# Kernel optimization log

Hardware: AMD Instinct MI355X
Metric: run time of the kernel (lower is better)

Reference implementation:

```python
import jax, jax.numpy as jnp
from jax import lax
import numpy as np

INPUT_SIZE = 32
HIDDEN = 128
FC1 = 64
OUT = 1
BATCH = 1024
SEQ = 512


def _lstm_layer(x, w_ih, w_hh, b_ih, b_hh):
    """Single PyTorch-convention LSTM layer (batch_first). x: [B,T,I] -> [B,T,H].
    Gate order in the 4H dim is (i, f, g, o), matching nn.LSTM."""
    B = x.shape[0]
    H = w_hh.shape[1]
    # Precompute input contribution for all timesteps (big GEMM, done once).
    gx = jnp.einsum('bti,gi->btg', x, w_ih) + b_ih + b_hh  # [B,T,4H]
    gx_t = jnp.swapaxes(gx, 0, 1)  # [T,B,4H] for scan over time

    def step(carry, gxt):
        h, c = carry
        gates = gxt + h @ w_hh.T  # [B,4H]
        i, f, g, o = jnp.split(gates, 4, axis=-1)
        i = jax.nn.sigmoid(i)
        f = jax.nn.sigmoid(f)
        g = jnp.tanh(g)
        o = jax.nn.sigmoid(o)
        c = f * c + i * g
        h = o * jnp.tanh(c)
        return (h, c), h

    h0 = jnp.zeros((B, H), dtype=x.dtype)
    c0 = jnp.zeros((B, H), dtype=x.dtype)
    (_, _), hs = lax.scan(step, (h0, c0), gx_t)
    return jnp.swapaxes(hs, 0, 1)  # [B,T,H]


def setup_inputs() -> dict:
    key = jax.random.key(0)
    ks = jax.random.split(key, 16)
    s_in = 1.0 / np.sqrt(HIDDEN)  # PyTorch LSTM init scale
    inp = {
        'x': jax.random.normal(ks[0], (BATCH, SEQ, INPUT_SIZE), dtype=jnp.float32),
        # LSTM layer 0
        'w_ih0': jax.random.uniform(ks[1], (4 * HIDDEN, INPUT_SIZE), minval=-s_in, maxval=s_in),
        'w_hh0': jax.random.uniform(ks[2], (4 * HIDDEN, HIDDEN), minval=-s_in, maxval=s_in),
        'b_ih0': jax.random.uniform(ks[3], (4 * HIDDEN,), minval=-s_in, maxval=s_in),
        'b_hh0': jax.random.uniform(ks[4], (4 * HIDDEN,), minval=-s_in, maxval=s_in),
        # LSTM layer 1
        'w_ih1': jax.random.uniform(ks[5], (4 * HIDDEN, HIDDEN), minval=-s_in, maxval=s_in),
        'w_hh1': jax.random.uniform(ks[6], (4 * HIDDEN, HIDDEN), minval=-s_in, maxval=s_in),
        'b_ih1': jax.random.uniform(ks[7], (4 * HIDDEN,), minval=-s_in, maxval=s_in),
        'b_hh1': jax.random.uniform(ks[8], (4 * HIDDEN,), minval=-s_in, maxval=s_in),
        # FC head
        'fc1_w': jax.random.uniform(ks[9], (FC1, HIDDEN), minval=-s_in, maxval=s_in),
        'fc1_b': jax.random.uniform(ks[10], (FC1,), minval=-s_in, maxval=s_in),
        'fc2_w': jax.random.uniform(ks[11], (OUT, FC1), minval=-1.0 / np.sqrt(FC1), maxval=1.0 / np.sqrt(FC1)),
        'fc2_b': jax.random.uniform(ks[12], (OUT,), minval=-1.0 / np.sqrt(FC1), maxval=1.0 / np.sqrt(FC1)),
    }
    return inp


def reference(x, w_ih0, w_hh0, b_ih0, b_hh0, w_ih1, w_hh1, b_ih1, b_hh1,
              fc1_w, fc1_b, fc2_w, fc2_b):
    # 2-layer LSTM (inter-layer dropout disabled: eval/inference mode)
    h1 = _lstm_layer(x, w_ih0, w_hh0, b_ih0, b_hh0)   # [B,T,H]
    h2 = _lstm_layer(h1, w_ih1, w_hh1, b_ih1, b_hh1)  # [B,T,H]
    last = h2[:, -1, :]                                # [B,H]
    out = jax.nn.relu(last @ fc1_w.T + fc1_b)          # [B,64]; dropout = identity (eval)
    out = out @ fc2_w.T + fc2_b                        # [B,1]
    return out
```

## Files before the change

### kernel.cpp

```cpp
#include <hip/hip_runtime.h>

#define HID   128
#define SEQL  512
#define MT    16
#define TPB   512
#define BATCH 1024

typedef __attribute__((ext_vector_type(4))) float    f32x4;
typedef __attribute__((ext_vector_type(8))) _Float16 f16x8;

union Pack8 { int2 p2[2]; int4 p4; f16x8 h; _Float16 hf[8]; short s[8]; };

__device__ __forceinline__ short f2hs(float f) {
    _Float16 v = (_Float16)f;
    return __builtin_bit_cast(short, v);
}
__device__ __forceinline__ float fsig(float x) {
    return __builtin_amdgcn_rcpf(1.f + __expf(-x));
}
__device__ __forceinline__ float ftanh(float x) {
    return 1.f - 2.f * __builtin_amdgcn_rcpf(1.f + __expf(2.f * x));
}

__global__ void prep_kernel(const float* __restrict__ x,
                            const float* __restrict__ w_ih0, const float* __restrict__ w_hh0,
                            const float* __restrict__ b_ih0, const float* __restrict__ b_hh0,
                            const float* __restrict__ w_ih1, const float* __restrict__ w_hh1,
                            const float* __restrict__ b_ih1, const float* __restrict__ b_hh1,
                            short* __restrict__ recW0, short* __restrict__ recW1,
                            short* __restrict__ inW1, short* __restrict__ xW0,
                            float* __restrict__ bias0, float* __restrict__ bias1,
                            short* __restrict__ xf) {
    int tid = blockIdx.x * 256 + threadIdx.x;
    if (tid < 2097152) {
        int g4 = tid & 3, c = (tid >> 2) & 15, t = (tid >> 6) & 511, grp = tid >> 15;
        const float* src = x + ((size_t)(grp * 16 + c) * 512 + t) * 32 + g4 * 8;
        Pack8 p;
        #pragma unroll
        for (int i = 0; i < 8; ++i) p.hf[i] = (_Float16)src[i];
        *(int4*)(xf + (size_t)tid * 8) = p.p4;
    } else if (tid < 2121728) {
        int q = tid - 2097152;
        int m = q >> 13;
        int r = q & 8191;
        int lane = r & 63, kk = (r >> 6) & 3, g = (r >> 8) & 3, w = r >> 10;
        int c = lane & 15, g4 = lane >> 4;
        int col = g * 128 + w * 16 + c;
        const float* src = (m == 0) ? w_hh0 : (m == 1) ? w_hh1 : w_ih1;
        short* dst = ((m == 0) ? recW0 : (m == 1) ? recW1 : inW1) + (size_t)r * 8;
        #pragma unroll
        for (int i = 0; i < 8; ++i)
            dst[i] = f2hs(src[col * 128 + kk * 32 + 8 * g4 + i]);
    } else if (tid < 2123776) {
        int r = tid - 2121728;
        int lane = r & 63, g = (r >> 6) & 3, w = r >> 8;
        int c = lane & 15, g4 = lane >> 4;
        int col = g * 128 + w * 16 + c;
        short* dst = xW0 + (size_t)r * 8;
        #pragma unroll
        for (int i = 0; i < 8; ++i)
            dst[i] = f2hs(w_ih0[col * 32 + 8 * g4 + i]);
    } else if (tid < 2124288) {
        int j = tid - 2123776;
        bias0[j] = b_ih0[j] + b_hh0[j];
    } else if (tid < 2124800) {
        int j = tid - 2124288;
        bias1[j] = b_ih1[j] + b_hh1[j];
    }
}

__global__ __launch_bounds__(TPB, 2) void fused_lstm_kernel(
    const short* __restrict__ xf,
    const short* __restrict__ recW0g, const short* __restrict__ recW1g,
    const short* __restrict__ inW1g,  const short* __restrict__ xW0g,
    const float* __restrict__ bias0,  const float* __restrict__ bias1,
    const float* __restrict__ fc1_w, const float* __restrict__ fc1_b,
    const float* __restrict__ fc2_w, const float* __restrict__ fc2_b,
    float* __restrict__ out)
{
    extern __shared__ char smem[];
    short* inL = (short*)smem;
    char*  hS0 = smem + 131072;
    char*  hS1 = smem + 139264;

    const int tid = threadIdx.x;
    const int w = tid >> 6, lane = tid & 63;
    const int c = lane & 15, g4 = lane >> 4;
    const int row0 = blockIdx.x * MT;

    #pragma unroll
    for (int i = 0; i < 32; ++i)
        ((int4*)inL)[i * TPB + tid] = ((const int4*)inW1g)[i * TPB + tid];
    #pragma unroll
    for (int i = 0; i < 8; ++i)
        ((int*)hS0)[i * TPB + tid] = 0;

    Pack8 recW0f[4][4], recW1f[4][4], xWf[4];
    #pragma unroll
    for (int g = 0; g < 4; ++g)
        #pragma unroll
        for (int kk = 0; kk < 4; ++kk) {
            recW0f[g][kk].p4 = *(const int4*)(recW0g + (size_t)((((w*4+g)*4+kk)*64 + lane) * 8));
            recW1f[g][kk].p4 = *(const int4*)(recW1g + (size_t)((((w*4+g)*4+kk)*64 + lane) * 8));
        }
    #pragma unroll
    for (int g = 0; g < 4; ++g)
        xWf[g].p4 = *(const int4*)(xW0g + (size_t)(((w*4+g)*64 + lane) * 8));

    float biasr0[4], biasr1[4];
    #pragma unroll
    for (int g = 0; g < 4; ++g) {
        biasr0[g] = bias0[g*128 + w*16 + c];
        biasr1[g] = bias1[g*128 + w*16 + c];
    }

    __syncthreads();

    float cst0[4] = {0.f, 0.f, 0.f, 0.f};
    float cst1[4] = {0.f, 0.f, 0.f, 0.f};

    const short* xfp = xf + (size_t)blockIdx.x * 262144 + c * 32 + g4 * 8;

    const int swz   = (c & 14) << 3;
    const int rbase = c * 256;
    const int unit  = w * 16 + c;
    int woff[4];
    #pragma unroll
    for (int r = 0; r < 4; ++r) {
        int rrow = 4 * g4 + r;
        woff[r] = rrow * 256 + ((unit * 2) ^ ((rrow & 14) << 3));
    }
    const int inBbase = w * 16384;

    Pack8 xv, xn;
    xv.p4 = *(const int4*)(xfp);
    xn.p4 = *(const int4*)(xfp + 512);

    {
        Pack8 ah0[4];
        #pragma unroll
        for (int kk = 0; kk < 4; ++kk)
            ah0[kk].p4 = *(const int4*)(hS0 + (rbase + ((kk*64 + 16*g4) ^ swz)));
        f32x4 acc0[4];
        #pragma unroll
        for (int g = 0; g < 4; ++g) { float b = biasr0[g]; acc0[g] = (f32x4){b,b,b,b}; }
        #pragma unroll
        for (int g = 0; g < 4; ++g)
            acc0[g] = __builtin_amdgcn_mfma_f32_16x16x32_f16(xv.h, xWf[g].h, acc0[g], 0, 0, 0);
        #pragma unroll
        for (int kk = 0; kk < 4; ++kk)
            #pragma unroll
            for (int g = 0; g < 4; ++g)
                acc0[g] = __builtin_amdgcn_mfma_f32_16x16x32_f16(ah0[kk].h, recW0f[g][kk].h, acc0[g], 0, 0, 0);
        char* h0w = hS0 + 4096;
        #pragma unroll
        for (int r = 0; r < 4; ++r) {
            float si = fsig(acc0[0][r]), sf = fsig(acc0[1][r]);
            float tg = ftanh(acc0[2][r]), so = fsig(acc0[3][r]);
            float cc = sf * cst0[r] + si * tg;
            cst0[r] = cc;
            float hh = so * ftanh(cc);
            *(_Float16*)(h0w + woff[r]) = (_Float16)hh;
        }
        __syncthreads();
    }

    for (int t = 1; t < SEQL; ++t) {
        const int rb = t & 1;
        const char* h0r = hS0 + rb * 4096;
        const char* h1r = hS1 + rb * 4096;
        char* h0w = hS0 + (rb ^ 1) * 4096;
        char* h1w = hS1 + (rb ^ 1) * 4096;

        xv = xn;
        int tn = (t + 1 < SEQL) ? t + 1 : SEQL - 1;
        xn.p4 = *(const int4*)(xfp + (size_t)tn * 512);

        Pack8 ah0[4], ah1[4];
        #pragma unroll
        for (int kk = 0; kk < 4; ++kk) {
            ah0[kk].p4 = *(const int4*)(h0r + (rbase + ((kk*64 + 16*g4) ^ swz)));
            ah1[kk].p4 = *(const int4*)(h1r + (rbase + ((kk*64 + 16*g4) ^ swz)));
        }

        __builtin_amdgcn_s_setprio(1);
        f32x4 acc0[4];
        #pragma unroll
        for (int g = 0; g < 4; ++g) { float b = biasr0[g]; acc0[g] = (f32x4){b,b,b,b}; }
        #pragma unroll
        for (int g = 0; g < 4; ++g)
            acc0[g] = __builtin_amdgcn_mfma_f32_16x16x32_f16(xv.h, xWf[g].h, acc0[g], 0, 0, 0);
        #pragma unroll
        for (int kk = 0; kk < 4; ++kk)
            #pragma unroll
            for (int g = 0; g < 4; ++g)
                acc0[g] = __builtin_amdgcn_mfma_f32_16x16x32_f16(ah0[kk].h, recW0f[g][kk].h, acc0[g], 0, 0, 0);

        f32x4 acc1[4];
        #pragma unroll
        for (int g = 0; g < 4; ++g) { float b = biasr1[g]; acc1[g] = (f32x4){b,b,b,b}; }
        #pragma unroll
        for (int kk = 0; kk < 4; ++kk)
            #pragma unroll
            for (int g = 0; g < 4; ++g) {
                Pack8 bB;
                bB.p4 = *(const int4*)(smem + inBbase + (g*4 + kk)*1024 + lane*16);
                acc1[g] = __builtin_amdgcn_mfma_f32_16x16x32_f16(ah0[kk].h, bB.h, acc1[g], 0, 0, 0);
            }

        #pragma unroll
        for (int kk = 0; kk < 4; ++kk) {
            #pragma unroll
            for (int g = 0; g < 4; ++g)
                acc1[g] = __builtin_amdgcn_mfma_f32_16x16x32_f16(ah1[kk].h, recW1f[g][kk].h, acc1[g], 0, 0, 0);
            float si = fsig(acc0[0][kk]), sf = fsig(acc0[1][kk]);
            float tg = ftanh(acc0[2][kk]), so = fsig(acc0[3][kk]);
            float cc = sf * cst0[kk] + si * tg;
            cst0[kk] = cc;
            float hh = so * ftanh(cc);
            *(_Float16*)(h0w + woff[kk]) = (_Float16)hh;
        }
        __builtin_amdgcn_s_setprio(0);

        #pragma unroll
        for (int r = 0; r < 4; ++r) {
            float si = fsig(acc1[0][r]), sf = fsig(acc1[1][r]);
            float tg = ftanh(acc1[2][r]), so = fsig(acc1[3][r]);
            float cc = sf * cst1[r] + si * tg;
            cst1[r] = cc;
            float hh = so * ftanh(cc);
            *(_Float16*)(h1w + woff[r]) = (_Float16)hh;
        }
        __syncthreads();
    }

    {
        const char* h0r = hS0;
        const char* h1r = hS1;
        Pack8 ah0[4], ah1[4];
        #pragma unroll
        for (int kk = 0; kk < 4; ++kk) {
            ah0[kk].p4 = *(const int4*)(h0r + (rbase + ((kk*64 + 16*g4) ^ swz)));
            ah1[kk].p4 = *(const int4*)(h1r + (rbase + ((kk*64 + 16*g4) ^ swz)));
        }
        f32x4 acc1[4];
        #pragma unroll
        for (int g = 0; g < 4; ++g) { float b = biasr1[g]; acc1[g] = (f32x4){b,b,b,b}; }
        #pragma unroll
        for (int kk = 0; kk < 4; ++kk)
            #pragma unroll
            for (int g = 0; g < 4; ++g) {
                Pack8 bB;
                bB.p4 = *(const int4*)(smem + inBbase + (g*4 + kk)*1024 + lane*16);
                acc1[g] = __builtin_amdgcn_mfma_f32_16x16x32_f16(ah0[kk].h, bB.h, acc1[g], 0, 0, 0);
            }
        #pragma unroll
        for (int kk = 0; kk < 4; ++kk)
            #pragma unroll
            for (int g = 0; g < 4; ++g)
                acc1[g] = __builtin_amdgcn_mfma_f32_16x16x32_f16(ah1[kk].h, recW1f[g][kk].h, acc1[g], 0, 0, 0);
        __syncthreads();
        float* lastH = (float*)smem;
        #pragma unroll
        for (int r = 0; r < 4; ++r) {
            float si = fsig(acc1[0][r]), sf = fsig(acc1[1][r]);
            float tg = ftanh(acc1[2][r]), so = fsig(acc1[3][r]);
            float cc = sf * cst1[r] + si * tg;
            float hh = so * ftanh(cc);
            lastH[(4*g4 + r) * HID + unit] = hh;
        }
        __syncthreads();
        float* fcb = (float*)(smem + 8192);
        #pragma unroll
        for (int s = 0; s < 2; ++s) {
            int task = tid + s * TPB;
            int r = task >> 6, o = task & 63;
            float a = fc1_b[o];
            for (int k = 0; k < HID; ++k) a += lastH[r * HID + k] * fc1_w[o * HID + k];
            fcb[r * 64 + o] = fmaxf(a, 0.f);
        }
        __syncthreads();
        if (tid < MT) {
            float a = fc2_b[0];
            for (int k = 0; k < 64; ++k) a += fcb[tid * 64 + k] * fc2_w[k];
            out[row0 + tid] = a;
        }
    }
}

extern "C" void kernel_launch(void* const* d_in, const int* in_sizes, int n_in,
                              void* d_out, int out_size, void* d_ws, size_t ws_size,
                              hipStream_t stream) {
    const float* x     = (const float*)d_in[0];
    const float* w_ih0 = (const float*)d_in[1];
    const float* w_hh0 = (const float*)d_in[2];
    const float* b_ih0 = (const float*)d_in[3];
    const float* b_hh0 = (const float*)d_in[4];
    const float* w_ih1 = (const float*)d_in[5];
    const float* w_hh1 = (const float*)d_in[6];
    const float* b_ih1 = (const float*)d_in[7];
    const float* b_hh1 = (const float*)d_in[8];
    const float* fc1_w = (const float*)d_in[9];
    const float* fc1_b = (const float*)d_in[10];
    const float* fc2_w = (const float*)d_in[11];
    const float* fc2_b = (const float*)d_in[12];

    char* ws = (char*)d_ws;
    short* recW0 = (short*)(ws);
    short* recW1 = (short*)(ws + (128u << 10));
    short* inW1  = (short*)(ws + (256u << 10));
    short* xW0   = (short*)(ws + (384u << 10));
    float* bias0 = (float*)(ws + (416u << 10));
    float* bias1 = (float*)(ws + (418u << 10));
    short* xf    = (short*)(ws + (1u << 20));

    static bool attr_set = false;
    if (!attr_set) {
        hipFuncSetAttribute((const void*)fused_lstm_kernel,
                            hipFuncAttributeMaxDynamicSharedMemorySize, 147456);
        attr_set = true;
    }

    prep_kernel<<<8300, 256, 0, stream>>>(x, w_ih0, w_hh0, b_ih0, b_hh0,
                                          w_ih1, w_hh1, b_ih1, b_hh1,
                                          recW0, recW1, inW1, xW0, bias0, bias1, xf);
    fused_lstm_kernel<<<64, TPB, 147456, stream>>>(xf, recW0, recW1, inW1, xW0,
                                                   bias0, bias1,
                                                   fc1_w, fc1_b, fc2_w, fc2_b,
                                                   (float*)d_out);
}
```

Before: 1.363 ms.

## Split LSTM layers across separate wave groups in a 1024-thread block

Doubles the block to 1024 threads and assigns waves 0-7 to layer 0 and waves 8-15 to layer 1, instead of each wave computing both layers per timestep. Each wave now keeps only one layer's recurrent weights in registers, which lowers register pressure, and the two layers' MFMA chains run in parallel on different waves. Occupancy drops to one block per CU because launch bounds no longer request 2 blocks, and the setprio hints are removed. Both groups still meet at a barrier every timestep.

```diff
diff --git a/kernel.cpp b/kernel.cpp
--- a/kernel.cpp
+++ b/kernel.cpp
@@ -3,7 +3,7 @@
 #define HID   128
 #define SEQL  512
 #define MT    16
-#define TPB   512
+#define TPB   1024
 #define BATCH 1024
 
 typedef __attribute__((ext_vector_type(4))) float    f32x4;
@@ -69,7 +69,7 @@
     }
 }
 
-__global__ __launch_bounds__(TPB, 2) void fused_lstm_kernel(
+__global__ __launch_bounds__(TPB) void fused_lstm_kernel(
     const short* __restrict__ xf,
     const short* __restrict__ recW0g, const short* __restrict__ recW1g,
     const short* __restrict__ inW1g,  const short* __restrict__ xW0g,
@@ -84,40 +84,46 @@
     char*  hS1 = smem + 139264;
 
     const int tid = threadIdx.x;
-    const int w = tid >> 6, lane = tid & 63;
+    const int wv = tid >> 6, lane = tid & 63;
     const int c = lane & 15, g4 = lane >> 4;
+    const int w = wv & 7;
+    const bool isL0 = (wv < 8);
     const int row0 = blockIdx.x * MT;
 
     #pragma unroll
-    for (int i = 0; i < 32; ++i)
+    for (int i = 0; i < 16; ++i)
         ((int4*)inL)[i * TPB + tid] = ((const int4*)inW1g)[i * TPB + tid];
     #pragma unroll
-    for (int i = 0; i < 8; ++i)
+    for (int i = 0; i < 4; ++i)
         ((int*)hS0)[i * TPB + tid] = 0;
 
-    Pack8 recW0f[4][4], recW1f[4][4], xWf[4];
-    #pragma unroll
-    for (int g = 0; g < 4; ++g)
-        #pragma unroll
-        for (int kk = 0; kk < 4; ++kk) {
-            recW0f[g][kk].p4 = *(const int4*)(recW0g + (size_t)((((w*4+g)*4+kk)*64 + lane) * 8));
-            recW1f[g][kk].p4 = *(const int4*)(recW1g + (size_t)((((w*4+g)*4+kk)*64 + lane) * 8));
-        }
-    #pragma unroll
-    for (int g = 0; g < 4; ++g)
-        xWf[g].p4 = *(const int4*)(xW0g + (size_t)(((w*4+g)*64 + lane) * 8));
-
-    float biasr0[4], biasr1[4];
-    #pragma unroll
-    for (int g = 0; g < 4; ++g) {
-        biasr0[g] = bias0[g*128 + w*16 + c];
-        biasr1[g] = bias1[g*128 + w*16 + c];
-    }
-
-    __syncthreads();
-
-    float cst0[4] = {0.f, 0.f, 0.f, 0.f};
-    float cst1[4] = {0.f, 0.f, 0.f, 0.f};
+    Pack8 recf[4][4];
+    Pack8 xWf[4];
+    float biasr[4];
+    if (isL0) {
+        #pragma unroll
+        for (int g = 0; g < 4; ++g)
+            #pragma unroll
+            for (int kk = 0; kk < 4; ++kk)
+                recf[g][kk].p4 = *(const int4*)(recW0g + (size_t)((((w*4+g)*4+kk)*64 + lane) * 8));
+        #pragma unroll
+        for (int g = 0; g < 4; ++g)
+            xWf[g].p4 = *(const int4*)(xW0g + (size_t)(((w*4+g)*64 + lane) * 8));
+        #pragma unroll
+        for (int g = 0; g < 4; ++g) biasr[g] = bias0[g*128 + w*16 + c];
+    } else {
+        #pragma unroll
+        for (int g = 0; g < 4; ++g)
+            #pragma unroll
+            for (int kk = 0; kk < 4; ++kk)
+                recf[g][kk].p4 = *(const int4*)(recW1g + (size_t)((((w*4+g)*4+kk)*64 + lane) * 8));
+        #pragma unroll
+        for (int g = 0; g < 4; ++g) biasr[g] = bias1[g*128 + w*16 + c];
+    }
+
+    __syncthreads();
+
+    float cst[4] = {0.f, 0.f, 0.f, 0.f};
 
     const short* xfp = xf + (size_t)blockIdx.x * 262144 + c * 32 + g4 * 8;
 
@@ -132,159 +138,158 @@
     }
     const int inBbase = w * 16384;
 
-    Pack8 xv, xn;
-    xv.p4 = *(const int4*)(xfp);
-    xn.p4 = *(const int4*)(xfp + 512);
-
-    {
-        Pack8 ah0[4];
-        #pragma unroll
-        for (int kk = 0; kk < 4; ++kk)
-            ah0[kk].p4 = *(const int4*)(hS0 + (rbase + ((kk*64 + 16*g4) ^ swz)));
-        f32x4 acc0[4];
-        #pragma unroll
-        for (int g = 0; g < 4; ++g) { float b = biasr0[g]; acc0[g] = (f32x4){b,b,b,b}; }
+    Pack8 xv;
+    if (isL0) xv.p4 = *(const int4*)(xfp);
+
+    if (isL0) {
+        f32x4 acc[4];
+        #pragma unroll
+        for (int g = 0; g < 4; ++g) { float b = biasr[g]; acc[g] = (f32x4){b,b,b,b}; }
         #pragma unroll
         for (int g = 0; g < 4; ++g)
-            acc0[g] = __builtin_amdgcn_mfma_f32_16x16x32_f16(xv.h, xWf[g].h, acc0[g], 0, 0, 0);
-        #pragma unroll
-        for (int kk = 0; kk < 4; ++kk)
+            acc[g] = __builtin_amdgcn_mfma_f32_16x16x32_f16(xv.h, xWf[g].h, acc[g], 0, 0, 0);
+        xv.p4 = *(const int4*)(xfp + 512);
+        #pragma unroll
+        for (int kk = 0; kk < 4; ++kk) {
+            Pack8 a;
+            a.p4 = *(const int4*)(hS0 + (rbase + ((kk*64 + 16*g4) ^ swz)));
             #pragma unroll
             for (int g = 0; g < 4; ++g)
-                acc0[g] = __builtin_amdgcn_mfma_f32_16x16x32_f16(ah0[kk].h, recW0f[g][kk].h, acc0[g], 0, 0, 0);
+                acc[g] = __builtin_amdgcn_mfma_f32_16x16x32_f16(a.h, recf[g][kk].h, acc[g], 0, 0, 0);
+        }
         char* h0w = hS0 + 4096;
         #pragma unroll
         for (int r = 0; r < 4; ++r) {
-            float si = fsig(acc0[0][r]), sf = fsig(acc0[1][r]);
-            float tg = ftanh(acc0[2][r]), so = fsig(acc0[3][r]);
-            float cc = sf * cst0[r] + si * tg;
-            cst0[r] = cc;
+            float si = fsig(acc[0][r]), sf = fsig(acc[1][r]);
+            float tg = ftanh(acc[2][r]), so = fsig(acc[3][r]);
+            float cc = sf * cst[r] + si * tg;
+            cst[r] = cc;
             float hh = so * ftanh(cc);
             *(_Float16*)(h0w + woff[r]) = (_Float16)hh;
         }
-        __syncthreads();
-    }
+    }
+    __syncthreads();
 
     for (int t = 1; t < SEQL; ++t) {
         const int rb = t & 1;
-        const char* h0r = hS0 + rb * 4096;
-        const char* h1r = hS1 + rb * 4096;
-        char* h0w = hS0 + (rb ^ 1) * 4096;
-        char* h1w = hS1 + (rb ^ 1) * 4096;
-
-        xv = xn;
-        int tn = (t + 1 < SEQL) ? t + 1 : SEQL - 1;
-        xn.p4 = *(const int4*)(xfp + (size_t)tn * 512);
-
-        Pack8 ah0[4], ah1[4];
+        if (isL0) {
+            const char* h0r = hS0 + rb * 4096;
+            char* h0w = hS0 + (rb ^ 1) * 4096;
+            f32x4 acc[4];
+            #pragma unroll
+            for (int g = 0; g < 4; ++g) { float b = biasr[g]; acc[g] = (f32x4){b,b,b,b}; }
+            #pragma unroll
+            for (int g = 0; g < 4; ++g)
+                acc[g] = __builtin_amdgcn_mfma_f32_16x16x32_f16(xv.h, xWf[g].h, acc[g], 0, 0, 0);
+            int tn = (t + 1 < SEQL) ? t + 1 : SEQL - 1;
+            xv.p4 = *(const int4*)(xfp + (size_t)tn * 512);
+            #pragma unroll
+            for (int kk = 0; kk < 4; ++kk) {
+                Pack8 a;
+                a.p4 = *(const int4*)(h0r + (rbase + ((kk*64 + 16*g4) ^ swz)));
+                #pragma unroll
+                for (int g = 0; g < 4; ++g)
+                    acc[g] = __builtin_amdgcn_mfma_f32_16x16x32_f16(a.h, recf[g][kk].h, acc[g], 0, 0, 0);
+            }
+            #pragma unroll
+            for (int r = 0; r < 4; ++r) {
+                float si = fsig(acc[0][r]), sf = fsig(acc[1][r]);
+                float tg = ftanh(acc[2][r]), so = fsig(acc[3][r]);
+                float cc = sf * cst[r] + si * tg;
+                cst[r] = cc;
+                float hh = so * ftanh(cc);
+                *(_Float16*)(h0w + woff[r]) = (_Float16)hh;
+            }
+        } else {
+            const char* h0r = hS0 + rb * 4096;
+            const char* h1r = hS1 + rb * 4096;
+            char* h1w = hS1 + (rb ^ 1) * 4096;
+            f32x4 acc[4];
+            #pragma unroll
+            for (int g = 0; g < 4; ++g) { float b = biasr[g]; acc[g] = (f32x4){b,b,b,b}; }
+            #pragma unroll
+            for (int kk = 0; kk < 4; ++kk) {
+                Pack8 a0;
+                a0.p4 = *(const int4*)(h0r + (rbase + ((kk*64 + 16*g4) ^ swz)));
+                #pragma unroll
+                for (int g = 0; g < 4; ++g) {
+                    Pack8 bB;
+                    bB.p4 = *(const int4*)(smem + inBbase + (g*4 + kk)*1024 + lane*16);
+                    acc[g] = __builtin_amdgcn_mfma_f32_16x16x32_f16(a0.h, bB.h, acc[g], 0, 0, 0);
+                }
+            }
+            #pragma unroll
+            for (int kk = 0; kk < 4; ++kk) {
+                Pack8 a1;
+                a1.p4 = *(const int4*)(h1r + (rbase + ((kk*64 + 16*g4) ^ swz)));
+                #pragma unroll
+                for (int g = 0; g < 4; ++g)
+                    acc[g] = __builtin_amdgcn_mfma_f32_16x16x32_f16(a1.h, recf[g][kk].h, acc[g], 0, 0, 0);
+            }
+            #pragma unroll
+            for (int r = 0; r < 4; ++r) {
+                float si = fsig(acc[0][r]), sf = fsig(acc[1][r]);
+                float tg = ftanh(acc[2][r]), so = fsig(acc[3][r]);
+                float cc = sf * cst[r] + si * tg;
+                cst[r] = cc;
+                float hh = so * ftanh(cc);
+                *(_Float16*)(h1w + woff[r]) = (_Float16)hh;
+            }
+        }
+        __syncthreads();
+    }
+
+    f32x4 accE[4];
+    if (!isL0) {
+        const char* h0r = hS0;
+        const char* h1r = hS1;
+        #pragma unroll
+        for (int g = 0; g < 4; ++g) { float b = biasr[g]; accE[g] = (f32x4){b,b,b,b}; }
         #pragma unroll
         for (int kk = 0; kk < 4; ++kk) {
-            ah0[kk].p4 = *(const int4*)(h0r + (rbase + ((kk*64 + 16*g4) ^ swz)));
-            ah1[kk].p4 = *(const int4*)(h1r + (rbase + ((kk*64 + 16*g4) ^ swz)));
-        }
-
-        __builtin_amdgcn_s_setprio(1);
-        f32x4 acc0[4];
-        #pragma unroll
-        for (int g = 0; g < 4; ++g) { float b = biasr0[g]; acc0[g] = (f32x4){b,b,b,b}; }
-        #pragma unroll
-        for (int g = 0; g < 4; ++g)
-            acc0[g] = __builtin_amdgcn_mfma_f32_16x16x32_f16(xv.h, xWf[g].h, acc0[g], 0, 0, 0);
-        #pragma unroll
-        for (int kk = 0; kk < 4; ++kk)
-            #pragma unroll
-            for (int g = 0; g < 4; ++g)
-                acc0[g] = __builtin_amdgcn_mfma_f32_16x16x32_f16(ah0[kk].h, recW0f[g][kk].h, acc0[g], 0, 0, 0);
-
-        f32x4 acc1[4];
-        #pragma unroll
-        for (int g = 0; g < 4; ++g) { float b = biasr1[g]; acc1[g] = (f32x4){b,b,b,b}; }
-        #pragma unroll
-        for (int kk = 0; kk < 4; ++kk)
+            Pack8 a0;
+            a0.p4 = *(const int4*)(h0r + (rbase + ((kk*64 + 16*g4) ^ swz)));
             #pragma unroll
             for (int g = 0; g < 4; ++g) {
                 Pack8 bB;
                 bB.p4 = *(const int4*)(smem + inBbase + (g*4 + kk)*1024 + lane*16);
-                acc1[g] = __builtin_amdgcn_mfma_f32_16x16x32_f16(ah0[kk].h, bB.h, acc1[g], 0, 0, 0);
-            }
-
+                accE[g] = __builtin_amdgcn_mfma_f32_16x16x32_f16(a0.h, bB.h, accE[g], 0, 0, 0);
+            }
+        }
         #pragma unroll
         for (int kk = 0; kk < 4; ++kk) {
+            Pack8 a1;
+            a1.p4 = *(const int4*)(h1r + (rbase + ((kk*64 + 16*g4) ^ swz)));
             #pragma unroll
             for (int g = 0; g < 4; ++g)
-                acc1[g] = __builtin_amdgcn_mfma_f32_16x16x32_f16(ah1[kk].h, recW1f[g][kk].h, acc1[g], 0, 0, 0);
-            float si = fsig(acc0[0][kk]), sf = fsig(acc0[1][kk]);
-            float tg = ftanh(acc0[2][kk]), so = fsig(acc0[3][kk]);
-            float cc = sf * cst0[kk] + si * tg;
-            cst0[kk] = cc;
-            float hh = so * ftanh(cc);
-            *(_Float16*)(h0w + woff[kk]) = (_Float16)hh;
-        }
-        __builtin_amdgcn_s_setprio(0);
-
+                accE[g] = __builtin_amdgcn_mfma_f32_16x16x32_f16(a1.h, recf[g][kk].h, accE[g], 0, 0, 0);
+        }
+    }
+    __syncthreads();
+    float* lastH = (float*)smem;
+    if (!isL0) {
         #pragma unroll
         for (int r = 0; r < 4; ++r) {
-            float si = fsig(acc1[0][r]), sf = fsig(acc1[1][r]);
-            float tg = ftanh(acc1[2][r]), so = fsig(acc1[3][r]);
-            float cc = sf * cst1[r] + si * tg;
-            cst1[r] = cc;
-            float hh = so * ftanh(cc);
-            *(_Float16*)(h1w + woff[r]) = (_Float16)hh;
-        }
-        __syncthreads();
-    }
-
-    {
-        const char* h0r = hS0;
-        const char* h1r = hS1;
-        Pack8 ah0[4], ah1[4];
-        #pragma unroll
-        for (int kk = 0; kk < 4; ++kk) {
-            ah0[kk].p4 = *(const int4*)(h0r + (rbase + ((kk*64 + 16*g4) ^ swz)));
-            ah1[kk].p4 = *(const int4*)(h1r + (rbase + ((kk*64 + 16*g4) ^ swz)));
-        }
-        f32x4 acc1[4];
-        #pragma unroll
-        for (int g = 0; g < 4; ++g) { float b = biasr1[g]; acc1[g] = (f32x4){b,b,b,b}; }
-        #pragma unroll
-        for (int kk = 0; kk < 4; ++kk)
-            #pragma unroll
-            for (int g = 0; g < 4; ++g) {
-                Pack8 bB;
-                bB.p4 = *(const int4*)(smem + inBbase + (g*4 + kk)*1024 + lane*16);
-                acc1[g] = __builtin_amdgcn_mfma_f32_16x16x32_f16(ah0[kk].h, bB.h, acc1[g], 0, 0, 0);
-            }
-        #pragma unroll
-        for (int kk = 0; kk < 4; ++kk)
-            #pragma unroll
-            for (int g = 0; g < 4; ++g)
-                acc1[g] = __builtin_amdgcn_mfma_f32_16x16x32_f16(ah1[kk].h, recW1f[g][kk].h, acc1[g], 0, 0, 0);
-        __syncthreads();
-        float* lastH = (float*)smem;
-        #pragma unroll
-        for (int r = 0; r < 4; ++r) {
-            float si = fsig(acc1[0][r]), sf = fsig(acc1[1][r]);
-            float tg = ftanh(acc1[2][r]), so = fsig(acc1[3][r]);
-            float cc = sf * cst1[r] + si * tg;
+            float si = fsig(accE[0][r]), sf = fsig(accE[1][r]);
+            float tg = ftanh(accE[2][r]), so = fsig(accE[3][r]);
+            float cc = sf * cst[r] + si * tg;
             float hh = so * ftanh(cc);
             lastH[(4*g4 + r) * HID + unit] = hh;
         }
-        __syncthreads();
-        float* fcb = (float*)(smem + 8192);
-        #pragma unroll
-        for (int s = 0; s < 2; ++s) {
-            int task = tid + s * TPB;
-            int r = task >> 6, o = task & 63;
-            float a = fc1_b[o];
-            for (int k = 0; k < HID; ++k) a += lastH[r * HID + k] * fc1_w[o * HID + k];
-            fcb[r * 64 + o] = fmaxf(a, 0.f);
-        }
-        __syncthreads();
-        if (tid < MT) {
-            float a = fc2_b[0];
-            for (int k = 0; k < 64; ++k) a += fcb[tid * 64 + k] * fc2_w[k];
-            out[row0 + tid] = a;
-        }
+    }
+    __syncthreads();
+    float* fcb = (float*)(smem + 8192);
+    {
+        int r = tid >> 6, o = tid & 63;
+        float a = fc1_b[o];
+        for (int k = 0; k < HID; ++k) a += lastH[r * HID + k] * fc1_w[o * HID + k];
+        fcb[r * 64 + o] = fmaxf(a, 0.f);
+    }
+    __syncthreads();
+    if (tid < MT) {
+        float a = fc2_b[0];
+        for (int k = 0; k < 64; ++k) a += fcb[tid * 64 + k] * fc2_w[k];
+        out[row0 + tid] = a;
     }
 }
 
```

Result: faster. 1.317 ms (-3.3%).
